# Performance work log

Measured on AMD Instinct MI355X. Metric: run time of the kernel, lower is better.

The kernel has to match this reference:

```python
import jax, jax.numpy as jnp
import numpy as np
import itertools

EPS = 1e-5
SCALE = 16 ** -0.5  # key_dim ** -0.5
H_HEADS, KEY_DIM, D, RES, RES_, STRIDE = 8, 16, 32, 28, 14, 2


def hardswish(x):
    return x * jnp.clip(x + 3.0, 0.0, 6.0) / 6.0


def conv_bn_hw(x, w, g, b, m, v):
    # 1x1 conv (no bias) + eval-mode BatchNorm + Hardswish
    y = jnp.einsum('bchw,oc->bohw', x, w)
    scale = (g / jnp.sqrt(v + EPS))[:, None, None]
    y = (y - m[:, None, None]) * scale + b[:, None, None]
    return hardswish(y)


def _bias_idxs():
    offsets, idxs = {}, []
    for p1 in itertools.product(range(RES_), repeat=2):
        for p2 in itertools.product(range(RES), repeat=2):
            off = (abs(p1[0] * STRIDE - p2[0]), abs(p1[1] * STRIDE - p2[1]))
            if off not in offsets:
                offsets[off] = len(offsets)
            idxs.append(offsets[off])
    return np.array(idxs, dtype=np.int32).reshape(RES_ * RES_, RES * RES), len(offsets)


def setup_inputs() -> dict:
    key = jax.random.key(0)
    ks = jax.random.split(key, 8)
    B, C = 64, 256
    idxs, n_off = _bias_idxs()

    def bn_params(k, n):
        k1, k2, k3, k4 = jax.random.split(k, 4)
        return (jax.random.normal(k1, (n,)) * 0.1 + 1.0,
                jax.random.normal(k2, (n,)) * 0.1,
                jax.random.normal(k3, (n,)) * 0.1,
                jax.random.uniform(k4, (n,), minval=0.5, maxval=1.5))

    kv_g, kv_b, kv_m, kv_v = bn_params(ks[1], 384)
    q_g, q_b, q_m, q_v = bn_params(ks[2], 128)
    p_g, p_b, p_m, p_v = bn_params(ks[3], 512)
    return dict(
        x=jax.random.normal(ks[0], (B, C, 28, 28), dtype=jnp.float32),
        kv_w=jax.random.normal(ks[4], (384, C)) * 0.05,
        kv_g=kv_g, kv_b=kv_b, kv_m=kv_m, kv_v=kv_v,
        q_w=jax.random.normal(ks[5], (128, C)) * 0.05,
        q_g=q_g, q_b=q_b, q_m=q_m, q_v=q_v,
        proj_w=jax.random.normal(ks[6], (512, 256)) * 0.05,
        proj_g=p_g, proj_b=p_b, proj_m=p_m, proj_v=p_v,
        ab=jax.random.normal(ks[7], (H_HEADS, n_off)) * 0.02,
        bias_idxs=jnp.asarray(idxs),
    )


def reference(x, kv_w, kv_g, kv_b, kv_m, kv_v, q_w, q_g, q_b, q_m, q_v,
              proj_w, proj_g, proj_b, proj_m, proj_v, ab, bias_idxs):
    B = x.shape[0]
    N, N_ = RES * RES, RES_ * RES_
    kv = conv_bn_hw(x, kv_w, kv_g, kv_b, kv_m, kv_v).reshape(B, H_HEADS, KEY_DIM + D, N)
    k, v = kv[:, :, :KEY_DIM], kv[:, :, KEY_DIM:]
    # AvgPool2d(kernel=1, stride=2) == strided slice
    q = conv_bn_hw(x[:, :, ::STRIDE, ::STRIDE], q_w, q_g, q_b, q_m, q_v)
    q = q.reshape(B, H_HEADS, KEY_DIM, N_)
    bias = ab[:, bias_idxs]  # gather -> [H, N_, N]
    attn = jax.nn.softmax(jnp.einsum('bhdn,bhdm->bhnm', q, k) * SCALE + bias, axis=-1)
    out = jnp.einsum('bhdm,bhnm->bhdn', v, attn).reshape(B, H_HEADS * D, RES_, RES_)
    return conv_bn_hw(hardswish(out), proj_w, proj_g, proj_b, proj_m, proj_v)
```

## Files before the change

kernel.cpp:

```cpp
#include <hip/hip_runtime.h>
#include <cstddef>
#include <cstdint>


#define SCALE_ATTN2 0.36067376f
#define LOG2E 1.44269504f
#define BN_EPS 1e-5f

typedef short s8v __attribute__((ext_vector_type(8)));
typedef short s4v __attribute__((ext_vector_type(4)));
typedef float f4v __attribute__((ext_vector_type(4)));

__device__ __forceinline__ float hswish(float y) {
    float t = fminf(fmaxf(y + 3.0f, 0.0f), 6.0f);
    return y * t * (1.0f / 6.0f);
}
__device__ __forceinline__ unsigned short bf16_rn(float f) {
    unsigned u = __float_as_uint(f);
    unsigned r = (u + 0x7FFFu + ((u >> 16) & 1u)) >> 16;
    return (unsigned short)r;
}
__device__ __forceinline__ float bf16_to_f(unsigned short h) {
    return __uint_as_float(((unsigned)h) << 16);
}
__device__ __forceinline__ void gload_lds16(const void* gsrc, void* ldsdst) {
    __builtin_amdgcn_global_load_lds(
        (const __attribute__((address_space(1))) unsigned int*)gsrc,
        (__attribute__((address_space(3))) unsigned int*)ldsdst, 16, 0, 0);
}

__global__ __launch_bounds__(256)
void wprep(const float* __restrict__ W, short* __restrict__ hi,
           short* __restrict__ lo, int n4)
{
    int i = blockIdx.x * 256 + threadIdx.x;
    int stride = gridDim.x * 256;
    for (; i < n4; i += stride) {
        float4 v = reinterpret_cast<const float4*>(W)[i];
        s4v h, l;
        unsigned short hh;
        hh = bf16_rn(v.x); h[0] = (short)hh; l[0] = (short)bf16_rn(v.x - bf16_to_f(hh));
        hh = bf16_rn(v.y); h[1] = (short)hh; l[1] = (short)bf16_rn(v.y - bf16_to_f(hh));
        hh = bf16_rn(v.z); h[2] = (short)hh; l[2] = (short)bf16_rn(v.z - bf16_to_f(hh));
        hh = bf16_rn(v.w); h[3] = (short)hh; l[3] = (short)bf16_rn(v.w - bf16_to_f(hh));
        reinterpret_cast<s4v*>(hi)[i] = h;
        reinterpret_cast<s4v*>(lo)[i] = l;
    }
}

__global__ __launch_bounds__(256)
void xprep(const float* __restrict__ x, short* __restrict__ xT)
{
    __shared__ float T[64][65];
    int nt = blockIdx.x, b = blockIdx.y;
    int n0 = nt * 64;
    const float* xb = x + (size_t)b * 256 * 784;
    int t = threadIdx.x;
    int cr = t >> 2, s = t & 3;

    for (int ct = 0; ct < 4; ++ct) {
        __syncthreads();
#pragma unroll
        for (int qq = 0; qq < 4; ++qq) {
            int n = n0 + s * 16 + qq * 4;
            float4 v = make_float4(0.f, 0.f, 0.f, 0.f);
            if (n + 3 < 784)
                v = *reinterpret_cast<const float4*>(&xb[(size_t)(ct * 64 + cr) * 784 + n]);
            *reinterpret_cast<float4*>(&T[cr][s * 16 + qq * 4]) = v;
        }
        __syncthreads();
        int r = cr;
        if (n0 + r < 784) {
            size_t tb = ((((size_t)b * 13 + nt) * 4 + ct) << 13);
            short* hiB = xT + tb;
            short* loB = xT + tb + 4096;
            s8v h0, h1, l0, l1;
#pragma unroll
            for (int j = 0; j < 8; ++j) {
                float f = T[s * 16 + j][r];
                unsigned short hh = bf16_rn(f);
                h0[j] = (short)hh; l0[j] = (short)bf16_rn(f - bf16_to_f(hh));
            }
#pragma unroll
            for (int j = 0; j < 8; ++j) {
                float f = T[s * 16 + 8 + j][r];
                unsigned short hh = bf16_rn(f);
                h1[j] = (short)hh; l1[j] = (short)bf16_rn(f - bf16_to_f(hh));
            }
            int sw = (r & 7) << 3;
            int base = r * 64;
            *reinterpret_cast<s8v*>(&hiB[base + ((s * 16) ^ sw)]) = h0;
            *reinterpret_cast<s8v*>(&hiB[base + ((s * 16 + 8) ^ sw)]) = h1;
            *reinterpret_cast<s8v*>(&loB[base + ((s * 16) ^ sw)]) = l0;
            *reinterpret_cast<s8v*>(&loB[base + ((s * 16 + 8) ^ sw)]) = l1;
        }
    }
}

__global__ __launch_bounds__(256)
void bias_kernel(const float* __restrict__ ab, const int* __restrict__ idxs,
                 unsigned short* __restrict__ biasF, int n_off)
{
    int i = blockIdx.x * 256 + threadIdx.x;
    if (i < 196 * 784) {
        int id = idxs[i];
        int n = i / 784, m = i - n * 784;
#pragma unroll
        for (int h = 0; h < 8; ++h)
            biasF[((size_t)h * 208 + n) * 784 + m] = bf16_rn(ab[h * n_off + id] * LOG2E);
    }
}

__global__ __launch_bounds__(256)
void gemm_kv(const short* __restrict__ xT,
             const short* __restrict__ Whi, const short* __restrict__ Wlo,
             const float* __restrict__ G, const float* __restrict__ Bb,
             const float* __restrict__ Mm, const float* __restrict__ Vv,
             short* __restrict__ Kthi, short* __restrict__ Ktlo,
             short* __restrict__ Vbf)
{
    __shared__ short Bt[2][64][64];
    __shared__ float scs[128], shs[128];

    int nt = blockIdx.x, oy = blockIdx.y, b = blockIdx.z;
    int oBase = oy * 128;
    int tid = threadIdx.x, w = tid >> 6, l = tid & 63;
    int fr = l & 15, g = l >> 4;

    if (tid < 128) {
        int o = oBase + tid;
        float sc = G[o] * rsqrtf(Vv[o] + BN_EPS);
        scs[tid] = sc; shs[tid] = Bb[o] - Mm[o] * sc;
    }

    f4v acc[2][4];
#pragma unroll
    for (int i = 0; i < 2; ++i)
#pragma unroll
        for (int j = 0; j < 4; ++j) acc[i][j] = (f4v)0.0f;

    const char* tilesrc = (const char*)(xT) + ((((size_t)b * 13 + nt) * 4) << 14);
    char* ldsbase = (char*)&Bt[0][0][0];

    for (int ct = 0; ct < 4; ++ct) {
        __syncthreads();
        {
            const char* src = tilesrc + ((size_t)ct << 14) + w * 4096 + l * 16;
            char* dst = ldsbase + w * 4096;
#pragma unroll
            for (int j = 0; j < 4; ++j)
                gload_lds16(src + j * 1024, dst + j * 1024);
        }
        __syncthreads();
#pragma unroll
        for (int ks = 0; ks < 2; ++ks) {
            s8v ah[2], al[2];
#pragma unroll
            for (int mf = 0; mf < 2; ++mf) {
                int o = oBase + w * 32 + mf * 16 + fr;
                size_t wi = (size_t)o * 256 + ct * 64 + ks * 32 + g * 8;
                ah[mf] = *reinterpret_cast<const s8v*>(&Whi[wi]);
                al[mf] = *reinterpret_cast<const s8v*>(&Wlo[wi]);
            }
#pragma unroll
            for (int nf = 0; nf < 4; ++nf) {
                int r = nf * 16 + fr;
                int ci = (ks * 32 + g * 8) ^ ((r & 7) << 3);
                s8v bh = *reinterpret_cast<const s8v*>(&Bt[0][r][ci]);
                s8v bl = *reinterpret_cast<const s8v*>(&Bt[1][r][ci]);
#pragma unroll
                for (int mf = 0; mf < 2; ++mf) {
                    acc[mf][nf] = __builtin_amdgcn_mfma_f32_16x16x32_bf16(ah[mf], bh, acc[mf][nf], 0, 0, 0);
                    acc[mf][nf] = __builtin_amdgcn_mfma_f32_16x16x32_bf16(ah[mf], bl, acc[mf][nf], 0, 0, 0);
                    acc[mf][nf] = __builtin_amdgcn_mfma_f32_16x16x32_bf16(al[mf], bh, acc[mf][nf], 0, 0, 0);
                }
            }
        }
    }

    int nBase = nt * 64;
#pragma unroll
    for (int mf = 0; mf < 2; ++mf) {
        int ol = w * 32 + mf * 16 + g * 4;
        int o = oBase + ol;
        int h = o / 48;
        int c = o - h * 48;
        if (c < 16) {
#pragma unroll
            for (int nf = 0; nf < 4; ++nf) {
                int n = nBase + nf * 16 + fr;
                if (n < 784) {
                    s4v hv, lv;
#pragma unroll
                    for (int e = 0; e < 4; ++e) {
                        float z = hswish(acc[mf][nf][e] * scs[ol + e] + shs[ol + e]);
                        unsigned short hh = bf16_rn(z);
                        hv[e] = (short)hh; lv[e] = (short)bf16_rn(z - bf16_to_f(hh));
                    }
                    size_t ki = (((size_t)b * 8 + h) * 784 + n) * 16 + c;
                    *reinterpret_cast<s4v*>(&Kthi[ki]) = hv;
                    *reinterpret_cast<s4v*>(&Ktlo[ki]) = lv;
                }
            }
        } else {
            int d = c - 16;
#pragma unroll
            for (int nf = 0; nf < 4; ++nf) {
                int n = nBase + nf * 16 + fr;
                if (n < 784) {
#pragma unroll
                    for (int e = 0; e < 4; ++e) {
                        float z = hswish(acc[mf][nf][e] * scs[ol + e] + shs[ol + e]);
                        Vbf[(((size_t)b * 8 + h) * 32 + d + e) * 784 + n] = (short)bf16_rn(z);
                    }
                }
            }
        }
    }
}

__global__ __launch_bounds__(256)
void gemm_q(const float* __restrict__ x,
            const short* __restrict__ Whi, const short* __restrict__ Wlo,
            const float* __restrict__ G, const float* __restrict__ Bb,
            const float* __restrict__ Mm, const float* __restrict__ Vv,
            short* __restrict__ Qthi, short* __restrict__ Qtlo)
{
    __shared__ short Bt[2][64][64];
    __shared__ float scs[128], shs[128];

    int nt = blockIdx.x, b = blockIdx.z;
    const float* xb = x + (size_t)b * 256 * 784;
    int tid = threadIdx.x, w = tid >> 6, l = tid & 63;
    int fr = l & 15, g = l >> 4;
    int sr = tid >> 4, sc4 = (tid & 15) * 4;

    if (tid < 128) {
        int o = tid;
        float sc = G[o] * rsqrtf(Vv[o] + BN_EPS);
        scs[tid] = sc; shs[tid] = Bb[o] - Mm[o] * sc;
    }

    f4v acc[2][4];
#pragma unroll
    for (int i = 0; i < 2; ++i)
#pragma unroll
        for (int j = 0; j < 4; ++j) acc[i][j] = (f4v)0.0f;

    for (int ct = 0; ct < 4; ++ct) {
        __syncthreads();
#pragma unroll
        for (int jc = 0; jc < 4; ++jc) {
            int c = sr + jc * 16;
#pragma unroll
            for (int e = 0; e < 4; ++e) {
                int nn = nt * 64 + sc4 + e;
                float v = 0.0f;
                if (nn < 196) {
                    int rr = nn / 14, cc = nn - rr * 14;
                    v = xb[(size_t)(ct * 64 + c) * 784 + rr * 56 + cc * 2];
                }
                int r = sc4 + e;
                int ci = c ^ ((r & 7) << 3);
                unsigned short hh = bf16_rn(v);
                Bt[0][r][ci] = (short)hh;
                Bt[1][r][ci] = (short)bf16_rn(v - bf16_to_f(hh));
            }
        }
        __syncthreads();
#pragma unroll
        for (int ks = 0; ks < 2; ++ks) {
            s8v ah[2], al[2];
#pragma unroll
            for (int mf = 0; mf < 2; ++mf) {
                int o = w * 32 + mf * 16 + fr;
                size_t wi = (size_t)o * 256 + ct * 64 + ks * 32 + g * 8;
                ah[mf] = *reinterpret_cast<const s8v*>(&Whi[wi]);
                al[mf] = *reinterpret_cast<const s8v*>(&Wlo[wi]);
            }
#pragma unroll
            for (int nf = 0; nf < 4; ++nf) {
                int r = nf * 16 + fr;
                int ci = (ks * 32 + g * 8) ^ ((r & 7) << 3);
                s8v bh = *reinterpret_cast<const s8v*>(&Bt[0][r][ci]);
                s8v bl = *reinterpret_cast<const s8v*>(&Bt[1][r][ci]);
#pragma unroll
                for (int mf = 0; mf < 2; ++mf) {
                    acc[mf][nf] = __builtin_amdgcn_mfma_f32_16x16x32_bf16(ah[mf], bh, acc[mf][nf], 0, 0, 0);
                    acc[mf][nf] = __builtin_amdgcn_mfma_f32_16x16x32_bf16(ah[mf], bl, acc[mf][nf], 0, 0, 0);
                    acc[mf][nf] = __builtin_amdgcn_mfma_f32_16x16x32_bf16(al[mf], bh, acc[mf][nf], 0, 0, 0);
                }
            }
        }
    }

#pragma unroll
    for (int mf = 0; mf < 2; ++mf) {
        int ol = w * 32 + mf * 16 + g * 4;
        int h = ol >> 4, d0 = ol & 15;
#pragma unroll
        for (int nf = 0; nf < 4; ++nf) {
            int n = nt * 64 + nf * 16 + fr;
            if (n < 196) {
                s4v hv, lv;
#pragma unroll
                for (int e = 0; e < 4; ++e) {
                    float z = hswish(acc[mf][nf][e] * scs[ol + e] + shs[ol + e]);
                    unsigned short hh = bf16_rn(z);
                    hv[e] = (short)hh; lv[e] = (short)bf16_rn(z - bf16_to_f(hh));
                }
                size_t qi = (((size_t)b * 8 + h) * 196 + n) * 16 + d0;
                *reinterpret_cast<s4v*>(&Qthi[qi]) = hv;
                *reinterpret_cast<s4v*>(&Qtlo[qi]) = lv;
            }
        }
    }
}

__global__ __launch_bounds__(256, 8)
void attn_mfma(const short* __restrict__ Kthi, const short* __restrict__ Ktlo,
               const short* __restrict__ Vbf,
               const short* __restrict__ Qthi, const short* __restrict__ Qtlo,
               const unsigned short* __restrict__ biasF, short* __restrict__ actT)
{
    __shared__ short Pl[4][16][72];

    int tid = threadIdx.x, w = tid >> 6, l = tid & 63;
    int idx = blockIdx.x * 4 + w;
    int bh = idx / 13, tile = idx - bh * 13;
    int b = bh >> 3, h = bh & 7;
    int g = l >> 4, fr = l & 15;

    const short* Kbase = ((g < 2) ? Kthi : Ktlo) + (size_t)bh * 784 * 16;
    const short* Vb = Vbf + (size_t)bh * 32 * 784;
    const short* Qh = Qthi + (size_t)bh * 196 * 16;
    const short* Ql = Qtlo + (size_t)bh * 196 * 16;
    int n = tile * 16 + fr;
    const unsigned short* bB = biasF + ((size_t)h * 208 + n) * 784;

    s8v qf1 = (s8v)0, qf2 = (s8v)0;
    if (n < 196) {
        qf1 = *reinterpret_cast<const s8v*>(&Qh[(size_t)n * 16 + (g & 1) * 8]);
        if (g < 2) qf2 = *reinterpret_cast<const s8v*>(&Ql[(size_t)n * 16 + g * 8]);
    }

    f4v Oa0 = (f4v)0.0f, Oa1 = (f4v)0.0f;
    float M = -1e30f, L = 0.0f;

#pragma unroll 1
    for (int ch = 0; ch < 13; ++ch) {
        int m0 = ch * 64;
        int subLim = (ch == 12) ? 1 : 4;
        int mlim = (ch == 12) ? 16 : 64;

        float s[4][4];
#pragma unroll
        for (int sub = 0; sub < 4; ++sub) {
            if (sub < subLim) {
                int mg = m0 + sub * 16 + fr;
                s8v af = *reinterpret_cast<const s8v*>(&Kbase[(size_t)mg * 16 + (g & 1) * 8]);
                f4v a = (f4v)0.0f;
                a = __builtin_amdgcn_mfma_f32_16x16x32_bf16(af, qf1, a, 0, 0, 0);
                a = __builtin_amdgcn_mfma_f32_16x16x32_bf16(af, qf2, a, 0, 0, 0);
                s4v bv = *reinterpret_cast<const s4v*>(&bB[m0 + sub * 16 + g * 4]);
#pragma unroll
                for (int e = 0; e < 4; ++e)
                    s[sub][e] = a[e] * SCALE_ATTN2 + bf16_to_f((unsigned short)bv[e]);
            } else {
#pragma unroll
                for (int e = 0; e < 4; ++e) s[sub][e] = -1e30f;
            }
        }

        float mx = fmaxf(fmaxf(fmaxf(s[0][0], s[0][1]), fmaxf(s[0][2], s[0][3])),
                         fmaxf(fmaxf(s[1][0], s[1][1]), fmaxf(s[1][2], s[1][3])));
        mx = fmaxf(mx, fmaxf(fmaxf(fmaxf(s[2][0], s[2][1]), fmaxf(s[2][2], s[2][3])),
                             fmaxf(fmaxf(s[3][0], s[3][1]), fmaxf(s[3][2], s[3][3]))));
        mx = fmaxf(mx, __shfl_xor(mx, 16));
        mx = fmaxf(mx, __shfl_xor(mx, 32));
        if (__any(mx > M + 8.0f)) {
            float Mn = fmaxf(M, mx);
            float corr = exp2f(M - Mn);
            L *= corr;
#pragma unroll
            for (int e = 0; e < 4; ++e) { Oa0[e] *= corr; Oa1[e] *= corr; }
            M = Mn;
        }

        float Ls = 0.0f;
#pragma unroll
        for (int sub = 0; sub < 4; ++sub) {
            float p[4];
#pragma unroll
            for (int e = 0; e < 4; ++e) {
                int mml = sub * 16 + g * 4 + e;
                float pv = exp2f(s[sub][e] - M);
                p[e] = (mml < mlim) ? pv : 0.0f;
                Ls += p[e];
            }
            unsigned w0, w1;
            asm("v_cvt_pk_bf16_f32 %0, %1, %2" : "=v"(w0) : "v"(p[0]), "v"(p[1]));
            asm("v_cvt_pk_bf16_f32 %0, %1, %2" : "=v"(w1) : "v"(p[2]), "v"(p[3]));
            int mb = sub * 16 + g * 4;
            *reinterpret_cast<unsigned*>(&Pl[w][fr][mb]) = w0;
            *reinterpret_cast<unsigned*>(&Pl[w][fr][mb + 2]) = w1;
        }
        Ls += __shfl_xor(Ls, 16);
        Ls += __shfl_xor(Ls, 32);
        L += Ls;

#pragma unroll
        for (int kc = 0; kc < 2; ++kc) {
            s8v pf = *reinterpret_cast<const s8v*>(&Pl[w][fr][kc * 32 + g * 8]);
            int mf0 = m0 + kc * 32 + g * 8;
            s8v v0 = (s8v)0, v1 = (s8v)0;
            if (mf0 + 8 <= 784) {
                v0 = *reinterpret_cast<const s8v*>(&Vb[(size_t)fr * 784 + mf0]);
                v1 = *reinterpret_cast<const s8v*>(&Vb[(size_t)(16 + fr) * 784 + mf0]);
            }
            Oa0 = __builtin_amdgcn_mfma_f32_16x16x32_bf16(v0, pf, Oa0, 0, 0, 0);
            Oa1 = __builtin_amdgcn_mfma_f32_16x16x32_bf16(v1, pf, Oa1, 0, 0, 0);
        }
    }

    if (n < 196) {
        float inv = 1.0f / L;
        int r = n & 63, ntl = n >> 6;
        int sw = (r & 7) << 3;
#pragma unroll
        for (int dt = 0; dt < 2; ++dt) {
            int c0 = h * 32 + dt * 16 + g * 4;
            f4v* Op = dt ? &Oa1 : &Oa0;
            s4v hv, lv;
#pragma unroll
            for (int e = 0; e < 4; ++e) {
                float z = hswish((*Op)[e] * inv);
                unsigned short hh = bf16_rn(z);
                hv[e] = (short)hh; lv[e] = (short)bf16_rn(z - bf16_to_f(hh));
            }
            int ct = c0 >> 6, c2 = c0 & 63;
            size_t tb = ((((size_t)b * 4 + ntl) * 4 + ct) << 13);
            int idx2 = r * 64 + (c2 ^ sw);
            *reinterpret_cast<s4v*>(&actT[tb + idx2]) = hv;
            *reinterpret_cast<s4v*>(&actT[tb + 4096 + idx2]) = lv;
        }
    }
}

__global__ __launch_bounds__(256)
void gemm_proj(const short* __restrict__ actT,
               const short* __restrict__ Whi, const short* __restrict__ Wlo,
               const float* __restrict__ G, const float* __restrict__ Bb,
               const float* __restrict__ Mm, const float* __restrict__ Vv,
               float* __restrict__ out)
{
    __shared__ short Bt[2][64][64];
    __shared__ float scs[128], shs[128];

    int nt = blockIdx.x, oy = blockIdx.y, b = blockIdx.z;
    int oBase = oy * 128;
    int tid = threadIdx.x, w = tid >> 6, l = tid & 63;
    int fr = l & 15, g = l >> 4;

    if (tid < 128) {
        int o = oBase + tid;
        float sc = G[o] * rsqrtf(Vv[o] + BN_EPS);
        scs[tid] = sc; shs[tid] = Bb[o] - Mm[o] * sc;
    }

    f4v acc[2][4];
#pragma unroll
    for (int i = 0; i < 2; ++i)
#pragma unroll
        for (int j = 0; j < 4; ++j) acc[i][j] = (f4v)0.0f;

    const char* tilesrc = (const char*)(actT) + ((((size_t)b * 4 + nt) * 4) << 14);
    char* ldsbase = (char*)&Bt[0][0][0];

    for (int ct = 0; ct < 4; ++ct) {
        __syncthreads();
        {
            const char* src = tilesrc + ((size_t)ct << 14) + w * 4096 + l * 16;
            char* dst = ldsbase + w * 4096;
#pragma unroll
            for (int j = 0; j < 4; ++j)
                gload_lds16(src + j * 1024, dst + j * 1024);
        }
        __syncthreads();
#pragma unroll
        for (int ks = 0; ks < 2; ++ks) {
            s8v ah[2], al[2];
#pragma unroll
            for (int mf = 0; mf < 2; ++mf) {
                int o = oBase + w * 32 + mf * 16 + fr;
                size_t wi = (size_t)o * 256 + ct * 64 + ks * 32 + g * 8;
                ah[mf] = *reinterpret_cast<const s8v*>(&Whi[wi]);
                al[mf] = *reinterpret_cast<const s8v*>(&Wlo[wi]);
            }
#pragma unroll
            for (int nf = 0; nf < 4; ++nf) {
                int r = nf * 16 + fr;
                int ci = (ks * 32 + g * 8) ^ ((r & 7) << 3);
                s8v bh = *reinterpret_cast<const s8v*>(&Bt[0][r][ci]);
                s8v bl = *reinterpret_cast<const s8v*>(&Bt[1][r][ci]);
#pragma unroll
                for (int mf = 0; mf < 2; ++mf) {
                    acc[mf][nf] = __builtin_amdgcn_mfma_f32_16x16x32_bf16(ah[mf], bh, acc[mf][nf], 0, 0, 0);
                    acc[mf][nf] = __builtin_amdgcn_mfma_f32_16x16x32_bf16(ah[mf], bl, acc[mf][nf], 0, 0, 0);
                    acc[mf][nf] = __builtin_amdgcn_mfma_f32_16x16x32_bf16(al[mf], bh, acc[mf][nf], 0, 0, 0);
                }
            }
        }
    }

#pragma unroll
    for (int mf = 0; mf < 2; ++mf) {
        int ol = w * 32 + mf * 16 + g * 4;
#pragma unroll
        for (int nf = 0; nf < 4; ++nf) {
            int n = nt * 64 + nf * 16 + fr;
            if (n < 196) {
#pragma unroll
                for (int e = 0; e < 4; ++e) {
                    float z = hswish(acc[mf][nf][e] * scs[ol + e] + shs[ol + e]);
                    out[((size_t)b * 512 + oBase + ol + e) * 196 + n] = z;
                }
            }
        }
    }
}

extern "C" void kernel_launch(void* const* d_in, const int* in_sizes, int n_in,
                              void* d_out, int out_size, void* d_ws, size_t ws_size,
                              hipStream_t stream) {
    const float* x      = (const float*)d_in[0];
    const float* kv_w   = (const float*)d_in[1];
    const float* kv_g   = (const float*)d_in[2];
    const float* kv_b   = (const float*)d_in[3];
    const float* kv_m   = (const float*)d_in[4];
    const float* kv_v   = (const float*)d_in[5];
    const float* q_w    = (const float*)d_in[6];
    const float* q_g    = (const float*)d_in[7];
    const float* q_b    = (const float*)d_in[8];
    const float* q_m    = (const float*)d_in[9];
    const float* q_v    = (const float*)d_in[10];
    const float* proj_w = (const float*)d_in[11];
    const float* proj_g = (const float*)d_in[12];
    const float* proj_b = (const float*)d_in[13];
    const float* proj_m = (const float*)d_in[14];
    const float* proj_v = (const float*)d_in[15];
    const float* ab     = (const float*)d_in[16];
    const int*   idxs   = (const int*)d_in[17];
    float* out = (float*)d_out;

    int n_off = in_sizes[16] / 8;

    char* p = (char*)d_ws;
    size_t off = 0;
    auto alloc = [&](size_t bytes) -> char* {
        char* r = p + off;
        off += (bytes + 255) & ~(size_t)255;
        return r;
    };
    short* Kthi = (short*)alloc((size_t)64 * 8 * 784 * 16 * 2);
    short* Ktlo = (short*)alloc((size_t)64 * 8 * 784 * 16 * 2);
    short* Vbf  = (short*)alloc((size_t)64 * 8 * 32 * 784 * 2);
    short* Qthi = (short*)alloc((size_t)64 * 8 * 196 * 16 * 2);
    short* Qtlo = (short*)alloc((size_t)64 * 8 * 196 * 16 * 2);
    unsigned short* biasF = (unsigned short*)alloc((size_t)8 * 208 * 784 * 2);
    short* Wkvh = (short*)alloc((size_t)384 * 256 * 2);
    short* Wkvl = (short*)alloc((size_t)384 * 256 * 2);
    short* Wqh  = (short*)alloc((size_t)128 * 256 * 2);
    short* Wql  = (short*)alloc((size_t)128 * 256 * 2);
    short* Wpjh = (short*)alloc((size_t)512 * 256 * 2);
    short* Wpjl = (short*)alloc((size_t)512 * 256 * 2);
    short* xT   = (short*)alloc((size_t)64 * 13 * 4 * 16384);
    short* actT = xT;

    wprep<<<dim3(64), 256, 0, stream>>>(kv_w, Wkvh, Wkvl, 384 * 256 / 4);
    wprep<<<dim3(64), 256, 0, stream>>>(q_w, Wqh, Wql, 128 * 256 / 4);
    wprep<<<dim3(64), 256, 0, stream>>>(proj_w, Wpjh, Wpjl, 512 * 256 / 4);
    xprep<<<dim3(13, 64), 256, 0, stream>>>(x, xT);
    bias_kernel<<<dim3((196 * 784 + 255) / 256), 256, 0, stream>>>(ab, idxs, biasF, n_off);
    gemm_kv<<<dim3(13, 3, 64), 256, 0, stream>>>(xT, Wkvh, Wkvl, kv_g, kv_b, kv_m, kv_v,
                                                 Kthi, Ktlo, Vbf);
    gemm_q<<<dim3(4, 1, 64), 256, 0, stream>>>(x, Wqh, Wql, q_g, q_b, q_m, q_v,
                                               Qthi, Qtlo);
    attn_mfma<<<dim3(512 * 13 / 4), 256, 0, stream>>>(Kthi, Ktlo, Vbf, Qthi, Qtlo, biasF, actT);
    gemm_proj<<<dim3(4, 4, 64), 256, 0, stream>>>(actT, Wpjh, Wpjl,
                                                  proj_g, proj_b, proj_m, proj_v, out);
}
```

Baseline: 387.7 us.

## Process two query tiles per wave in attention to reuse K and V loads

Each wave in the attention kernel now handles two 16-row query tiles (7 work items per batch-head instead of 13), so every K fragment and V fragment it loads feeds both tiles. This halves the K/V global traffic per query row and amortises loop overhead, at the cost of more registers (launch bounds relaxed from 8 to 4 waves per SIMD) and fewer waves overall. Blocks are remapped with an interleaved index, and the bias kernel now zero-fills the padded rows 196 to 207, which the last tile pair can touch.

```diff
diff --git a/kernel.cpp b/kernel.cpp
--- a/kernel.cpp
+++ b/kernel.cpp
@@ -102,12 +102,18 @@
                  unsigned short* __restrict__ biasF, int n_off)
 {
     int i = blockIdx.x * 256 + threadIdx.x;
-    if (i < 196 * 784) {
-        int id = idxs[i];
+    if (i < 208 * 784) {
         int n = i / 784, m = i - n * 784;
-#pragma unroll
-        for (int h = 0; h < 8; ++h)
-            biasF[((size_t)h * 208 + n) * 784 + m] = bf16_rn(ab[h * n_off + id] * LOG2E);
+        if (n < 196) {
+            int id = idxs[i];
+#pragma unroll
+            for (int h = 0; h < 8; ++h)
+                biasF[((size_t)h * 208 + n) * 784 + m] = bf16_rn(ab[h * n_off + id] * LOG2E);
+        } else {
+#pragma unroll
+            for (int h = 0; h < 8; ++h)
+                biasF[((size_t)h * 208 + n) * 784 + m] = 0;
+        }
     }
 }
 
@@ -317,35 +323,44 @@
     }
 }
 
-__global__ __launch_bounds__(256, 8)
+__global__ __launch_bounds__(256, 4)
 void attn_mfma(const short* __restrict__ Kthi, const short* __restrict__ Ktlo,
                const short* __restrict__ Vbf,
                const short* __restrict__ Qthi, const short* __restrict__ Qtlo,
                const unsigned short* __restrict__ biasF, short* __restrict__ actT)
 {
-    __shared__ short Pl[4][16][72];
+    __shared__ short Pl[4][2][16][72];
 
     int tid = threadIdx.x, w = tid >> 6, l = tid & 63;
-    int idx = blockIdx.x * 4 + w;
-    int bh = idx / 13, tile = idx - bh * 13;
+    int lb = (blockIdx.x & 7) * 112 + (blockIdx.x >> 3);
+    int idx = lb * 4 + w;
+    int bh = idx / 7, j = idx - bh * 7;
     int b = bh >> 3, h = bh & 7;
     int g = l >> 4, fr = l & 15;
+    bool two = (j < 6);
+    int n0 = (2 * j) * 16 + fr;
+    int n1 = two ? (n0 + 16) : n0;
 
     const short* Kbase = ((g < 2) ? Kthi : Ktlo) + (size_t)bh * 784 * 16;
     const short* Vb = Vbf + (size_t)bh * 32 * 784;
     const short* Qh = Qthi + (size_t)bh * 196 * 16;
     const short* Ql = Qtlo + (size_t)bh * 196 * 16;
-    int n = tile * 16 + fr;
-    const unsigned short* bB = biasF + ((size_t)h * 208 + n) * 784;
-
-    s8v qf1 = (s8v)0, qf2 = (s8v)0;
-    if (n < 196) {
-        qf1 = *reinterpret_cast<const s8v*>(&Qh[(size_t)n * 16 + (g & 1) * 8]);
-        if (g < 2) qf2 = *reinterpret_cast<const s8v*>(&Ql[(size_t)n * 16 + g * 8]);
-    }
-
-    f4v Oa0 = (f4v)0.0f, Oa1 = (f4v)0.0f;
-    float M = -1e30f, L = 0.0f;
+    const unsigned short* bB0 = biasF + ((size_t)h * 208 + n0) * 784;
+    const unsigned short* bB1 = biasF + ((size_t)h * 208 + n1) * 784;
+
+    s8v qA0 = (s8v)0, qB0 = (s8v)0, qA1 = (s8v)0, qB1 = (s8v)0;
+    if (n0 < 196) {
+        qA0 = *reinterpret_cast<const s8v*>(&Qh[(size_t)n0 * 16 + (g & 1) * 8]);
+        if (g < 2) qB0 = *reinterpret_cast<const s8v*>(&Ql[(size_t)n0 * 16 + g * 8]);
+    }
+    if (two) {
+        qA1 = *reinterpret_cast<const s8v*>(&Qh[(size_t)n1 * 16 + (g & 1) * 8]);
+        if (g < 2) qB1 = *reinterpret_cast<const s8v*>(&Ql[(size_t)n1 * 16 + g * 8]);
+    }
+
+    f4v O00 = (f4v)0.0f, O01 = (f4v)0.0f;
+    f4v O10 = (f4v)0.0f, O11 = (f4v)0.0f;
+    float M0 = -1e30f, L0 = 0.0f, M1 = -1e30f, L1 = 0.0f;
 
 #pragma unroll 1
     for (int ch = 0; ch < 13; ++ch) {
@@ -353,88 +368,167 @@
         int subLim = (ch == 12) ? 1 : 4;
         int mlim = (ch == 12) ? 16 : 64;
 
-        float s[4][4];
+        float s0[4][4], s1[4][4];
 #pragma unroll
         for (int sub = 0; sub < 4; ++sub) {
             if (sub < subLim) {
                 int mg = m0 + sub * 16 + fr;
                 s8v af = *reinterpret_cast<const s8v*>(&Kbase[(size_t)mg * 16 + (g & 1) * 8]);
-                f4v a = (f4v)0.0f;
-                a = __builtin_amdgcn_mfma_f32_16x16x32_bf16(af, qf1, a, 0, 0, 0);
-                a = __builtin_amdgcn_mfma_f32_16x16x32_bf16(af, qf2, a, 0, 0, 0);
-                s4v bv = *reinterpret_cast<const s4v*>(&bB[m0 + sub * 16 + g * 4]);
+                f4v a0 = (f4v)0.0f;
+                a0 = __builtin_amdgcn_mfma_f32_16x16x32_bf16(af, qA0, a0, 0, 0, 0);
+                a0 = __builtin_amdgcn_mfma_f32_16x16x32_bf16(af, qB0, a0, 0, 0, 0);
+                s4v bv0 = *reinterpret_cast<const s4v*>(&bB0[m0 + sub * 16 + g * 4]);
 #pragma unroll
                 for (int e = 0; e < 4; ++e)
-                    s[sub][e] = a[e] * SCALE_ATTN2 + bf16_to_f((unsigned short)bv[e]);
+                    s0[sub][e] = a0[e] * SCALE_ATTN2 + bf16_to_f((unsigned short)bv0[e]);
+                if (two) {
+                    f4v a1 = (f4v)0.0f;
+                    a1 = __builtin_amdgcn_mfma_f32_16x16x32_bf16(af, qA1, a1, 0, 0, 0);
+                    a1 = __builtin_amdgcn_mfma_f32_16x16x32_bf16(af, qB1, a1, 0, 0, 0);
+                    s4v bv1 = *reinterpret_cast<const s4v*>(&bB1[m0 + sub * 16 + g * 4]);
+#pragma unroll
+                    for (int e = 0; e < 4; ++e)
+                        s1[sub][e] = a1[e] * SCALE_ATTN2 + bf16_to_f((unsigned short)bv1[e]);
+                } else {
+#pragma unroll
+                    for (int e = 0; e < 4; ++e) s1[sub][e] = -1e30f;
+                }
             } else {
 #pragma unroll
-                for (int e = 0; e < 4; ++e) s[sub][e] = -1e30f;
-            }
-        }
-
-        float mx = fmaxf(fmaxf(fmaxf(s[0][0], s[0][1]), fmaxf(s[0][2], s[0][3])),
-                         fmaxf(fmaxf(s[1][0], s[1][1]), fmaxf(s[1][2], s[1][3])));
-        mx = fmaxf(mx, fmaxf(fmaxf(fmaxf(s[2][0], s[2][1]), fmaxf(s[2][2], s[2][3])),
-                             fmaxf(fmaxf(s[3][0], s[3][1]), fmaxf(s[3][2], s[3][3]))));
-        mx = fmaxf(mx, __shfl_xor(mx, 16));
-        mx = fmaxf(mx, __shfl_xor(mx, 32));
-        if (__any(mx > M + 8.0f)) {
-            float Mn = fmaxf(M, mx);
-            float corr = exp2f(M - Mn);
-            L *= corr;
-#pragma unroll
-            for (int e = 0; e < 4; ++e) { Oa0[e] *= corr; Oa1[e] *= corr; }
-            M = Mn;
-        }
-
-        float Ls = 0.0f;
-#pragma unroll
-        for (int sub = 0; sub < 4; ++sub) {
-            float p[4];
-#pragma unroll
-            for (int e = 0; e < 4; ++e) {
-                int mml = sub * 16 + g * 4 + e;
-                float pv = exp2f(s[sub][e] - M);
-                p[e] = (mml < mlim) ? pv : 0.0f;
-                Ls += p[e];
-            }
-            unsigned w0, w1;
-            asm("v_cvt_pk_bf16_f32 %0, %1, %2" : "=v"(w0) : "v"(p[0]), "v"(p[1]));
-            asm("v_cvt_pk_bf16_f32 %0, %1, %2" : "=v"(w1) : "v"(p[2]), "v"(p[3]));
-            int mb = sub * 16 + g * 4;
-            *reinterpret_cast<unsigned*>(&Pl[w][fr][mb]) = w0;
-            *reinterpret_cast<unsigned*>(&Pl[w][fr][mb + 2]) = w1;
-        }
-        Ls += __shfl_xor(Ls, 16);
-        Ls += __shfl_xor(Ls, 32);
-        L += Ls;
+                for (int e = 0; e < 4; ++e) { s0[sub][e] = -1e30f; s1[sub][e] = -1e30f; }
+            }
+        }
+
+        {
+            float mx = s0[0][0];
+#pragma unroll
+            for (int sub = 0; sub < 4; ++sub)
+#pragma unroll
+                for (int e = 0; e < 4; ++e) mx = fmaxf(mx, s0[sub][e]);
+            mx = fmaxf(mx, __shfl_xor(mx, 16));
+            mx = fmaxf(mx, __shfl_xor(mx, 32));
+            if (__any(mx > M0 + 8.0f)) {
+                float Mn = fmaxf(M0, mx);
+                float corr = exp2f(M0 - Mn);
+                L0 *= corr;
+#pragma unroll
+                for (int e = 0; e < 4; ++e) { O00[e] *= corr; O01[e] *= corr; }
+                M0 = Mn;
+            }
+            float Ls = 0.0f;
+#pragma unroll
+            for (int sub = 0; sub < 4; ++sub) {
+                float p[4];
+#pragma unroll
+                for (int e = 0; e < 4; ++e) {
+                    int mml = sub * 16 + g * 4 + e;
+                    float pv = exp2f(s0[sub][e] - M0);
+                    p[e] = (mml < mlim) ? pv : 0.0f;
+                    Ls += p[e];
+                }
+                unsigned w0, w1;
+                asm("v_cvt_pk_bf16_f32 %0, %1, %2" : "=v"(w0) : "v"(p[0]), "v"(p[1]));
+                asm("v_cvt_pk_bf16_f32 %0, %1, %2" : "=v"(w1) : "v"(p[2]), "v"(p[3]));
+                int mb = sub * 16 + g * 4;
+                *reinterpret_cast<unsigned*>(&Pl[w][0][fr][mb]) = w0;
+                *reinterpret_cast<unsigned*>(&Pl[w][0][fr][mb + 2]) = w1;
+            }
+            Ls += __shfl_xor(Ls, 16);
+            Ls += __shfl_xor(Ls, 32);
+            L0 += Ls;
+        }
+        if (two) {
+            float mx = s1[0][0];
+#pragma unroll
+            for (int sub = 0; sub < 4; ++sub)
+#pragma unroll
+                for (int e = 0; e < 4; ++e) mx = fmaxf(mx, s1[sub][e]);
+            mx = fmaxf(mx, __shfl_xor(mx, 16));
+            mx = fmaxf(mx, __shfl_xor(mx, 32));
+            if (__any(mx > M1 + 8.0f)) {
+                float Mn = fmaxf(M1, mx);
+                float corr = exp2f(M1 - Mn);
+                L1 *= corr;
+#pragma unroll
+                for (int e = 0; e < 4; ++e) { O10[e] *= corr; O11[e] *= corr; }
+                M1 = Mn;
+            }
+            float Ls = 0.0f;
+#pragma unroll
+            for (int sub = 0; sub < 4; ++sub) {
+                float p[4];
+#pragma unroll
+                for (int e = 0; e < 4; ++e) {
+                    int mml = sub * 16 + g * 4 + e;
+                    float pv = exp2f(s1[sub][e] - M1);
+                    p[e] = (mml < mlim) ? pv : 0.0f;
+                    Ls += p[e];
+                }
+                unsigned w0, w1;
+                asm("v_cvt_pk_bf16_f32 %0, %1, %2" : "=v"(w0) : "v"(p[0]), "v"(p[1]));
+                asm("v_cvt_pk_bf16_f32 %0, %1, %2" : "=v"(w1) : "v"(p[2]), "v"(p[3]));
+                int mb = sub * 16 + g * 4;
+                *reinterpret_cast<unsigned*>(&Pl[w][1][fr][mb]) = w0;
+                *reinterpret_cast<unsigned*>(&Pl[w][1][fr][mb + 2]) = w1;
+            }
+            Ls += __shfl_xor(Ls, 16);
+            Ls += __shfl_xor(Ls, 32);
+            L1 += Ls;
+        }
 
 #pragma unroll
         for (int kc = 0; kc < 2; ++kc) {
-            s8v pf = *reinterpret_cast<const s8v*>(&Pl[w][fr][kc * 32 + g * 8]);
             int mf0 = m0 + kc * 32 + g * 8;
             s8v v0 = (s8v)0, v1 = (s8v)0;
             if (mf0 + 8 <= 784) {
                 v0 = *reinterpret_cast<const s8v*>(&Vb[(size_t)fr * 784 + mf0]);
                 v1 = *reinterpret_cast<const s8v*>(&Vb[(size_t)(16 + fr) * 784 + mf0]);
             }
-            Oa0 = __builtin_amdgcn_mfma_f32_16x16x32_bf16(v0, pf, Oa0, 0, 0, 0);
-            Oa1 = __builtin_amdgcn_mfma_f32_16x16x32_bf16(v1, pf, Oa1, 0, 0, 0);
-        }
-    }
-
-    if (n < 196) {
-        float inv = 1.0f / L;
-        int r = n & 63, ntl = n >> 6;
+            s8v pf0 = *reinterpret_cast<const s8v*>(&Pl[w][0][fr][kc * 32 + g * 8]);
+            O00 = __builtin_amdgcn_mfma_f32_16x16x32_bf16(v0, pf0, O00, 0, 0, 0);
+            O01 = __builtin_amdgcn_mfma_f32_16x16x32_bf16(v1, pf0, O01, 0, 0, 0);
+            if (two) {
+                s8v pf1 = *reinterpret_cast<const s8v*>(&Pl[w][1][fr][kc * 32 + g * 8]);
+                O10 = __builtin_amdgcn_mfma_f32_16x16x32_bf16(v0, pf1, O10, 0, 0, 0);
+                O11 = __builtin_amdgcn_mfma_f32_16x16x32_bf16(v1, pf1, O11, 0, 0, 0);
+            }
+        }
+    }
+
+    if (n0 < 196) {
+        float inv = 1.0f / L0;
+        int r = n0 & 63, ntl = n0 >> 6;
         int sw = (r & 7) << 3;
 #pragma unroll
         for (int dt = 0; dt < 2; ++dt) {
             int c0 = h * 32 + dt * 16 + g * 4;
-            f4v* Op = dt ? &Oa1 : &Oa0;
+            f4v Ov = dt ? O01 : O00;
             s4v hv, lv;
 #pragma unroll
             for (int e = 0; e < 4; ++e) {
-                float z = hswish((*Op)[e] * inv);
+                float z = hswish(Ov[e] * inv);
+                unsigned short hh = bf16_rn(z);
+                hv[e] = (short)hh; lv[e] = (short)bf16_rn(z - bf16_to_f(hh));
+            }
+            int ct = c0 >> 6, c2 = c0 & 63;
+            size_t tb = ((((size_t)b * 4 + ntl) * 4 + ct) << 13);
+            int idx2 = r * 64 + (c2 ^ sw);
+            *reinterpret_cast<s4v*>(&actT[tb + idx2]) = hv;
+            *reinterpret_cast<s4v*>(&actT[tb + 4096 + idx2]) = lv;
+        }
+    }
+    if (two) {
+        float inv = 1.0f / L1;
+        int r = n1 & 63, ntl = n1 >> 6;
+        int sw = (r & 7) << 3;
+#pragma unroll
+        for (int dt = 0; dt < 2; ++dt) {
+            int c0 = h * 32 + dt * 16 + g * 4;
+            f4v Ov = dt ? O11 : O10;
+            s4v hv, lv;
+#pragma unroll
+            for (int e = 0; e < 4; ++e) {
+                float z = hswish(Ov[e] * inv);
                 unsigned short hh = bf16_rn(z);
                 hv[e] = (short)hh; lv[e] = (short)bf16_rn(z - bf16_to_f(hh));
             }
@@ -581,12 +675,12 @@
     wprep<<<dim3(64), 256, 0, stream>>>(q_w, Wqh, Wql, 128 * 256 / 4);
     wprep<<<dim3(64), 256, 0, stream>>>(proj_w, Wpjh, Wpjl, 512 * 256 / 4);
     xprep<<<dim3(13, 64), 256, 0, stream>>>(x, xT);
-    bias_kernel<<<dim3((196 * 784 + 255) / 256), 256, 0, stream>>>(ab, idxs, biasF, n_off);
+    bias_kernel<<<dim3((208 * 784 + 255) / 256), 256, 0, stream>>>(ab, idxs, biasF, n_off);
     gemm_kv<<<dim3(13, 3, 64), 256, 0, stream>>>(xT, Wkvh, Wkvl, kv_g, kv_b, kv_m, kv_v,
                                                  Kthi, Ktlo, Vbf);
     gemm_q<<<dim3(4, 1, 64), 256, 0, stream>>>(x, Wqh, Wql, q_g, q_b, q_m, q_v,
                                                Qthi, Qtlo);
-    attn_mfma<<<dim3(512 * 13 / 4), 256, 0, stream>>>(Kthi, Ktlo, Vbf, Qthi, Qtlo, biasF, actT);
+    attn_mfma<<<dim3(896), 256, 0, stream>>>(Kthi, Ktlo, Vbf, Qthi, Qtlo, biasF, actT);
     gemm_proj<<<dim3(4, 4, 64), 256, 0, stream>>>(actT, Wpjh, Wpjl,
                                                   proj_g, proj_b, proj_m, proj_v, out);
 }
```

Result: faster. 322.1 us (-16.9%).
